# Kernel tuning notes

Hardware: AMD Instinct MI355X
Metric: run time of the kernel (lower is better)

## Reference

```python
import jax, jax.numpy as jnp
import numpy as np

B, D, DEPTH, C = 8192, 2048, 10, 1000
NUM_INNER = 2 ** DEPTH - 1   # 1023
NUM_LEAVES = 2 ** DEPTH      # 1024


def setup_inputs() -> dict:
    key = jax.random.key(0)
    k1, k2, k3, k4 = jax.random.split(key, 4)
    x = jax.random.normal(k1, (B, D), dtype=jnp.float32)
    # scale weights like a typical init so sigmoid isn't fully saturated
    W = jax.random.normal(k2, (D, NUM_INNER), dtype=jnp.float32) * 0.02
    b = jax.random.normal(k3, (NUM_INNER,), dtype=jnp.float32) * 0.02
    leaf_dist = jax.random.normal(k4, (NUM_LEAVES, C), dtype=jnp.float32)
    return {"x": x, "W": W, "b": b, "leaf_dist": leaf_dist}


def reference(x, W, b, leaf_dist):
    # inner node routing probabilities: [B, num_inner]
    decisions = jax.nn.sigmoid(x @ W + b)
    depth = int(np.log2(decisions.shape[1] + 1))
    pp = jnp.ones((x.shape[0], 1), dtype=x.dtype)  # path probs, starts at root
    for d in range(depth):  # small fixed loop over tree depth
        s, e = 2 ** d - 1, 2 ** (d + 1) - 1
        ld = decisions[:, s:e]                      # [B, 2^d]
        pp = jnp.concatenate([pp * ld, pp * (1.0 - ld)], axis=1)  # [B, 2^(d+1)]
        # faithful reproduction of the original's even/odd reordering
        pp = jnp.concatenate([pp[:, ::2], pp[:, 1::2]], axis=1)
    leaf_probs = jax.nn.softmax(leaf_dist, axis=1)  # [num_leaves, C]
    return pp @ leaf_probs                          # [B, C]
```

## Files before the change

kernel.cpp:

```cpp
#include <hip/hip_runtime.h>

typedef __attribute__((ext_vector_type(8))) unsigned short ushort8v;
typedef __attribute__((ext_vector_type(8))) __bf16 bf16x8;
typedef __attribute__((ext_vector_type(4))) float floatx4;

__device__ __forceinline__ unsigned short f2b(float f) {
    unsigned u = __float_as_uint(f);
    unsigned r = u + 0x7fffu + ((u >> 16) & 1u);
    return (unsigned short)(r >> 16);
}
__device__ __forceinline__ float b2f(unsigned short h) {
    return __uint_as_float(((unsigned)h) << 16);
}

__device__ __forceinline__ void gload16(const unsigned short* g, unsigned short* l) {
    __builtin_amdgcn_global_load_lds(
        (const __attribute__((address_space(1))) unsigned int*)g,
        (__attribute__((address_space(3))) unsigned int*)l,
        16, 0, 0);
}


__global__ __launch_bounds__(256) void prep_kernel(const float* __restrict__ x,
                                                   unsigned short* __restrict__ A2x,
                                                   const float* __restrict__ W,
                                                   unsigned short* __restrict__ B2w,
                                                   const float* __restrict__ ld_,
                                                   unsigned short* __restrict__ B2p) {
    __shared__ float tile[32 * 33];
    __shared__ float buf[1000];
    __shared__ float red[8];
    const int b = blockIdx.x, t = threadIdx.x;
    if (b < 2048) {
        const int mt = b >> 2, kq = (b & 3) * 64;
        const int kco = t >> 4, l16 = t & 15;
        const float* xr0 = x + (size_t)(mt * 16 + l16) * 2048;
#pragma unroll
        for (int i = 0; i < 4; i++) {
            const int kc = kq + i * 16 + kco;
            const float* xr = xr0 + kc * 8;
            float4 v0 = *(const float4*)xr;
            float4 v1 = *(const float4*)(xr + 4);
            ushort8v o;
            o[0] = f2b(v0.x); o[1] = f2b(v0.y); o[2] = f2b(v0.z); o[3] = f2b(v0.w);
            o[4] = f2b(v1.x); o[5] = f2b(v1.y); o[6] = f2b(v1.z); o[7] = f2b(v1.w);
            *(ushort8v*)(A2x + ((size_t)(mt * 256 + kc) * 16 + l16) * 8) = o;
        }
    } else if (b < 4096) {
        const int idx = b - 2048;
        const int n0 = (idx & 31) * 32, k0 = (idx >> 5) * 32;
        const int tx = t & 31, ty = t >> 5;
#pragma unroll
        for (int i = 0; i < 4; i++) {
            int k = k0 + ty + i * 8, n = n0 + tx;
            tile[(ty + i * 8) * 33 + tx] = (n < 1023) ? W[(size_t)k * 1023 + n] : 0.f;
        }
        __syncthreads();
#pragma unroll
        for (int i = 0; i < 4; i++) {
            int n = n0 + ty + i * 8, k = k0 + tx;
            size_t off = ((size_t)((n >> 4) * 256 + (k >> 3)) * 16 + (n & 15)) * 8 + (k & 7);
            B2w[off] = f2b(tile[tx * 33 + ty + i * 8]);
        }
    } else {
        const int l0 = b - 4096;
        const float* r = ld_ + (size_t)l0 * 1000;
        float mx = -3.4e38f;
        for (int i = t; i < 1000; i += 256) { float v = r[i]; buf[i] = v; mx = fmaxf(mx, v); }
#pragma unroll
        for (int o = 32; o > 0; o >>= 1) mx = fmaxf(mx, __shfl_down(mx, o));
        if ((t & 63) == 0) red[t >> 6] = mx;
        __syncthreads();
        mx = fmaxf(fmaxf(red[0], red[1]), fmaxf(red[2], red[3]));
        float s = 0.f;
        for (int i = t; i < 1000; i += 256) { float e = __expf(buf[i] - mx); buf[i] = e; s += e; }
#pragma unroll
        for (int o = 32; o > 0; o >>= 1) s += __shfl_down(s, o);
        if ((t & 63) == 0) red[4 + (t >> 6)] = s;
        __syncthreads();
        float inv = 1.f / (red[4] + red[5] + red[6] + red[7]);
        for (int i = t; i < 1024; i += 256) {
            float pv = (i < 1000) ? buf[i] * inv : 0.f;
            size_t off = ((size_t)((i >> 4) * 128 + (l0 >> 3)) * 16 + (i & 15)) * 8 + (l0 & 7);
            B2p[off] = f2b(pv);
        }
    }
}

__global__ __launch_bounds__(256) void pp_kernel(const unsigned short* __restrict__ dec,
                                                 unsigned short* __restrict__ A2p) {
    __shared__ unsigned short dsh[8 * 1024];
    __shared__ float pa[8 * 1024];
    __shared__ float pb[8 * 1024];
    const int t = threadIdx.x;
    const int r0 = blockIdx.x * 8;
    {
        const ushort8v* src = (const ushort8v*)(dec + (size_t)r0 * 1024);
        ushort8v* dst = (ushort8v*)dsh;
        for (int g = t; g < 1024; g += 256) dst[g] = src[g];
    }
    if (t < 8) pa[t * 1024] = 1.f;
    __syncthreads();
    float* cur = pa; float* nxt = pb;
    for (int dep = 0; dep < 10; dep++) {
        const int half = 1 << dep;
        const int len  = half << 1;
        const int total = len << 3;
        for (int idx = t; idx < total; idx += 256) {
            const int r = idx >> (dep + 1);
            const int j = idx & (len - 1);
            int tt = j >> dep;
            int s  = j & (half - 1);
            int i2 = 2 * s + tt;
            int u  = i2 >> dep;
            int rr = i2 & (half - 1);
            float dv = b2f(dsh[r * 1024 + half - 1 + rr]);
            nxt[r * 1024 + j] = cur[r * 1024 + rr] * (u ? (1.f - dv) : dv);
        }
        __syncthreads();
        float* tmp = cur; cur = nxt; nxt = tmp;
    }
    for (int i = t; i < 8192; i += 256) {
        const int r = i >> 10, j = i & 1023;
        const int rrow = r0 + r;
        size_t off = ((size_t)((rrow >> 4) * 128 + (j >> 3)) * 16 + (rrow & 15)) * 8 + (j & 7);
        A2p[off] = f2b(cur[r * 1024 + j]);
    }
}

#define VMW(N) asm volatile("s_waitcnt vmcnt(" #N ")" ::: "memory")

#define P4_STEP(ks_, b_, VM_, DOSTAGE_)                                             \
    {                                                                               \
        VMW(VM_);                                                                   \
        __builtin_amdgcn_s_barrier();                                               \
        __builtin_amdgcn_sched_barrier(0);                                          \
        const unsigned short* lA = &lds[(b_)][0];                                   \
        const unsigned short* lB = &lds[(b_)][4096];                                \
        bf16x8 af[4], bv[4];                                                        \
        _Pragma("unroll")                                                           \
        for (int m2 = 0; m2 < 4; m2++)                                              \
            af[m2] = __builtin_bit_cast(bf16x8,                                     \
                *(const ushort8v*)&lA[((wr * 4 + m2) * 4 + quad) * 128 + l16 * 8]); \
        _Pragma("unroll")                                                           \
        for (int n2 = 0; n2 < 4; n2++)                                              \
            bv[n2] = __builtin_bit_cast(bf16x8,                                     \
                *(const ushort8v*)&lB[((wc * 4 + n2) * 4 + quad) * 128 + l16 * 8]); \
        asm volatile("s_waitcnt lgkmcnt(0)" ::: "memory");                          \
        __builtin_amdgcn_sched_barrier(0);                                          \
        __builtin_amdgcn_s_barrier();                                               \
        __builtin_amdgcn_sched_barrier(0);                                          \
        if (DOSTAGE_) STAGE((ks_) + 4, (b_));                                       \
        __builtin_amdgcn_s_setprio(1);                                              \
        _Pragma("unroll")                                                           \
        for (int m2 = 0; m2 < 4; m2++)                                              \
            _Pragma("unroll")                                                       \
            for (int n2 = 0; n2 < 4; n2++)                                          \
                acc[m2][n2] = __builtin_amdgcn_mfma_f32_16x16x32_bf16(              \
                    af[m2], bv[n2], acc[m2][n2], 0, 0, 0);                          \
        __builtin_amdgcn_s_setprio(0);                                              \
    }

template <int EPI, int KC>
__global__ __launch_bounds__(256, 2) void gemm_p4(const unsigned short* __restrict__ A2,
                                                  const unsigned short* __restrict__ B2,
                                                  const float* __restrict__ bias,
                                                  unsigned short* __restrict__ obf,
                                                  float* __restrict__ of32, int ldo) {
    __shared__ unsigned short lds[4][8192];

    const int tid  = threadIdx.x;
    const int lane = tid & 63;
    const int wave = tid >> 6;
    const int quad = lane >> 4, l16 = lane & 15;
    const int wr = wave >> 1, wc = wave & 1;

    const int bid = blockIdx.x;
    const int bn  = bid & 7;
    const int bm  = bid >> 3;

    const int c0  = tid >> 4;
    const int sub = (tid & 15) * 8;
    const unsigned short* gA0 = A2 + ((size_t)(bm * 8 + (c0 >> 2))        * KC + (c0 & 3)) * 128 + sub;
    const unsigned short* gA1 = A2 + ((size_t)(bm * 8 + ((c0 + 16) >> 2)) * KC + (c0 & 3)) * 128 + sub;
    const unsigned short* gB0 = B2 + ((size_t)(bn * 8 + (c0 >> 2))        * KC + (c0 & 3)) * 128 + sub;
    const unsigned short* gB1 = B2 + ((size_t)(bn * 8 + ((c0 + 16) >> 2)) * KC + (c0 & 3)) * 128 + sub;
    const int dA0 = c0 * 128 + sub;
    const int dA1 = (c0 + 16) * 128 + sub;
    const int dB0 = 4096 + c0 * 128 + sub;
    const int dB1 = 4096 + (c0 + 16) * 128 + sub;

    floatx4 acc[4][4] = {};
    constexpr int nks = KC / 4;

    auto STAGE = [&](int ks, int b) {
        const size_t ko = (size_t)ks * 512;
        gload16(gA0 + ko, &lds[b][dA0]);
        gload16(gA1 + ko, &lds[b][dA1]);
        gload16(gB0 + ko, &lds[b][dB0]);
        gload16(gB1 + ko, &lds[b][dB1]);
    };

    STAGE(0, 0); STAGE(1, 1); STAGE(2, 2); STAGE(3, 3);

    for (int ks = 0; ks < nks - 4; ++ks) {
        P4_STEP(ks, ks & 3, 12, true);
    }
    P4_STEP(nks - 4, (nks - 4) & 3, 12, false);
    P4_STEP(nks - 3, (nks - 3) & 3, 8,  false);
    P4_STEP(nks - 2, (nks - 2) & 3, 4,  false);
    P4_STEP(nks - 1, (nks - 1) & 3, 0,  false);

    const int mt0 = bm * 8 + wr * 4;
    const int nt0 = bn * 8 + wc * 4;
#pragma unroll
    for (int n2 = 0; n2 < 4; n2++) {
        const int col = (nt0 + n2) * 16 + l16;
        float bbias = 0.f;
        if constexpr (EPI == 0) bbias = (col < 1023) ? bias[col] : 0.f;
#pragma unroll
        for (int m2 = 0; m2 < 4; m2++) {
            const int row0 = (mt0 + m2) * 16 + quad * 4;
#pragma unroll
            for (int r = 0; r < 4; r++) {
                float v = acc[m2][n2][r];
                if constexpr (EPI == 0) {
                    float sgm = 1.f / (1.f + __expf(-(v + bbias)));
                    obf[(size_t)(row0 + r) * ldo + col] = f2b(sgm);
                } else {
                    if (col < 1000) of32[(size_t)(row0 + r) * ldo + col] = v;
                }
            }
        }
    }
}

extern "C" void kernel_launch(void* const* d_in, const int* in_sizes, int n_in,
                              void* d_out, int out_size, void* d_ws, size_t ws_size,
                              hipStream_t stream) {
    const float* x   = (const float*)d_in[0];
    const float* W   = (const float*)d_in[1];
    const float* b   = (const float*)d_in[2];
    const float* ldd = (const float*)d_in[3];
    float* out = (float*)d_out;

    char* ws = (char*)d_ws;
    unsigned short* A2x = (unsigned short*)(ws);
    unsigned short* A2p = (unsigned short*)(ws);
    unsigned short* B2w = (unsigned short*)(ws + 33554432);
    unsigned short* dec = (unsigned short*)(ws + 37748736);
    unsigned short* B2p = (unsigned short*)(ws + 54525952);

    prep_kernel<<<5120, 256, 0, stream>>>(x, A2x, W, B2w, ldd, B2p);
    gemm_p4<0, 256><<<512, 256, 0, stream>>>(A2x, B2w, b, dec, nullptr, 1024);
    pp_kernel<<<1024, 256, 0, stream>>>(dec, A2p);
    gemm_p4<1, 128><<<512, 256, 0, stream>>>(A2p, B2p, nullptr, nullptr, out, 1000);
}
```

Before: 210.3 us.

## Use 256x128 tile, 512-thread GEMM with triple buffering and XCD-aware block mapping

Replaces the first GEMM (x@W with sigmoid epilogue) with a new 512-thread kernel using 256x128 tiles and a three-stage LDS ring buffer, halving the grid to 256 blocks with one block per CU. Block indices are remapped so each XCD works on a contiguous group of M-tiles, which should improve L2 reuse of A. The second GEMM gets the same XCD-aware mapping and loses the unused sigmoid epilogue template. The aim is more operand reuse per LDS load and less global traffic. The trade-off is lower occupancy and a shallower prefetch pipeline.

```diff
diff --git a/kernel.cpp b/kernel.cpp
--- a/kernel.cpp
+++ b/kernel.cpp
@@ -13,7 +13,7 @@
     return __uint_as_float(((unsigned)h) << 16);
 }
 
-__device__ __forceinline__ void gload16(const unsigned short* g, unsigned short* l) {
+__device__ __forceinline__ void gload16(const void* g, void* l) {
     __builtin_amdgcn_global_load_lds(
         (const __attribute__((address_space(1))) unsigned int*)g,
         (__attribute__((address_space(3))) unsigned int*)l,
@@ -129,6 +129,102 @@
 }
 
 #define VMW(N) asm volatile("s_waitcnt vmcnt(" #N ")" ::: "memory")
+
+#define M1_STEP(ks_, CUR_, STG_, VM_, DOSTAGE_)                                       \
+    {                                                                                 \
+        if (DOSTAGE_) STAGE((ks_) + 2, (STG_));                                       \
+        VMW(VM_);                                                                     \
+        __builtin_amdgcn_s_barrier();                                                 \
+        const unsigned short* lA = &lds[(CUR_)][0];                                   \
+        const unsigned short* lB = &lds[(CUR_)][8192];                                \
+        bf16x8 af[4], bv[4];                                                          \
+        _Pragma("unroll")                                                             \
+        for (int m2 = 0; m2 < 4; m2++)                                                \
+            af[m2] = __builtin_bit_cast(bf16x8,                                       \
+                *(const ushort8v*)&lA[((wr * 4 + m2) * 4 + quad) * 128 + l16 * 8]);   \
+        _Pragma("unroll")                                                             \
+        for (int n2 = 0; n2 < 4; n2++)                                                \
+            bv[n2] = __builtin_bit_cast(bf16x8,                                       \
+                *(const ushort8v*)&lB[((wc * 4 + n2) * 4 + quad) * 128 + l16 * 8]);   \
+        asm volatile("s_waitcnt lgkmcnt(0)" ::: "memory");                            \
+        __builtin_amdgcn_sched_barrier(0);                                            \
+        __builtin_amdgcn_s_setprio(1);                                                \
+        _Pragma("unroll")                                                             \
+        for (int m2 = 0; m2 < 4; m2++)                                                \
+            _Pragma("unroll")                                                         \
+            for (int n2 = 0; n2 < 4; n2++)                                            \
+                acc[m2][n2] = __builtin_amdgcn_mfma_f32_16x16x32_bf16(                \
+                    af[m2], bv[n2], acc[m2][n2], 0, 0, 0);                            \
+        __builtin_amdgcn_s_setprio(0);                                                \
+        __builtin_amdgcn_s_barrier();                                                 \
+    }
+
+__global__ __launch_bounds__(512, 1) void gemm_m1(const unsigned short* __restrict__ A2,
+                                                  const unsigned short* __restrict__ B2,
+                                                  const float* __restrict__ bias,
+                                                  unsigned short* __restrict__ obf) {
+    constexpr int KC = 256;
+    __shared__ unsigned short lds[3][12288];
+
+    const int tid  = threadIdx.x;
+    const int lane = tid & 63;
+    const int wave = tid >> 6;
+    const int quad = lane >> 4, l16 = lane & 15;
+    const int wr = wave >> 1, wc = wave & 1;
+
+    const int bid = blockIdx.x;
+    const int xcd = bid & 7;
+    const int j   = bid >> 3;
+    const int bm  = xcd * 4 + (j & 3);
+    const int bn  = j >> 2;
+
+    const int cA  = tid >> 4;
+    const int sub = (tid & 15) * 8;
+    const unsigned short* gA0 = A2 + ((size_t)(bm * 16 + (cA >> 2))        * KC + (cA & 3)) * 128 + sub;
+    const unsigned short* gA1 = A2 + ((size_t)(bm * 16 + ((cA + 32) >> 2)) * KC + (cA & 3)) * 128 + sub;
+    const unsigned short* gB0 = B2 + ((size_t)(bn * 8  + (cA >> 2))        * KC + (cA & 3)) * 128 + sub;
+    const int dA0 = cA * 128 + sub;
+    const int dA1 = (cA + 32) * 128 + sub;
+    const int dB0 = 8192 + cA * 128 + sub;
+
+    floatx4 acc[4][4] = {};
+    constexpr int nks = KC / 4;
+
+    auto STAGE = [&](int ks, int b) {
+        const size_t ko = (size_t)ks * 512;
+        gload16(gA0 + ko, &lds[b][dA0]);
+        gload16(gA1 + ko, &lds[b][dA1]);
+        gload16(gB0 + ko, &lds[b][dB0]);
+    };
+
+    STAGE(0, 0); STAGE(1, 1);
+
+    int c0 = 0, c1 = 1, c2 = 2;
+    for (int ks = 0; ks < nks - 2; ++ks) {
+        M1_STEP(ks, c0, c2, 6, true);
+        int tmp = c0; c0 = c1; c1 = c2; c2 = tmp;
+    }
+    M1_STEP(nks - 2, c0, c2, 3, false);
+    { int tmp = c0; c0 = c1; c1 = c2; c2 = tmp; }
+    M1_STEP(nks - 1, c0, c2, 0, false);
+
+    const int mt0 = bm * 16 + wr * 4;
+    const int nt0 = bn * 8  + wc * 4;
+#pragma unroll
+    for (int n2 = 0; n2 < 4; n2++) {
+        const int col = (nt0 + n2) * 16 + l16;
+        const float bbias = (col < 1023) ? bias[col] : 0.f;
+#pragma unroll
+        for (int m2 = 0; m2 < 4; m2++) {
+            const int row0 = (mt0 + m2) * 16 + quad * 4;
+#pragma unroll
+            for (int r = 0; r < 4; r++) {
+                float sgm = 1.f / (1.f + __expf(-(acc[m2][n2][r] + bbias)));
+                obf[(size_t)(row0 + r) * 1024 + col] = f2b(sgm);
+            }
+        }
+    }
+}
 
 #define P4_STEP(ks_, b_, VM_, DOSTAGE_)                                             \
     {                                                                               \
@@ -161,11 +257,9 @@
         __builtin_amdgcn_s_setprio(0);                                              \
     }
 
-template <int EPI, int KC>
+template <int KC>
 __global__ __launch_bounds__(256, 2) void gemm_p4(const unsigned short* __restrict__ A2,
                                                   const unsigned short* __restrict__ B2,
-                                                  const float* __restrict__ bias,
-                                                  unsigned short* __restrict__ obf,
                                                   float* __restrict__ of32, int ldo) {
     __shared__ unsigned short lds[4][8192];
 
@@ -176,8 +270,10 @@
     const int wr = wave >> 1, wc = wave & 1;
 
     const int bid = blockIdx.x;
-    const int bn  = bid & 7;
-    const int bm  = bid >> 3;
+    const int xcd = bid & 7;
+    const int j   = bid >> 3;
+    const int bm  = xcd * 8 + (j & 7);
+    const int bn  = j >> 3;
 
     const int c0  = tid >> 4;
     const int sub = (tid & 15) * 8;
@@ -216,20 +312,12 @@
 #pragma unroll
     for (int n2 = 0; n2 < 4; n2++) {
         const int col = (nt0 + n2) * 16 + l16;
-        float bbias = 0.f;
-        if constexpr (EPI == 0) bbias = (col < 1023) ? bias[col] : 0.f;
 #pragma unroll
         for (int m2 = 0; m2 < 4; m2++) {
             const int row0 = (mt0 + m2) * 16 + quad * 4;
 #pragma unroll
             for (int r = 0; r < 4; r++) {
-                float v = acc[m2][n2][r];
-                if constexpr (EPI == 0) {
-                    float sgm = 1.f / (1.f + __expf(-(v + bbias)));
-                    obf[(size_t)(row0 + r) * ldo + col] = f2b(sgm);
-                } else {
-                    if (col < 1000) of32[(size_t)(row0 + r) * ldo + col] = v;
-                }
+                if (col < 1000) of32[(size_t)(row0 + r) * ldo + col] = acc[m2][n2][r];
             }
         }
     }
@@ -252,7 +340,7 @@
     unsigned short* B2p = (unsigned short*)(ws + 54525952);
 
     prep_kernel<<<5120, 256, 0, stream>>>(x, A2x, W, B2w, ldd, B2p);
-    gemm_p4<0, 256><<<512, 256, 0, stream>>>(A2x, B2w, b, dec, nullptr, 1024);
+    gemm_m1<<<256, 512, 0, stream>>>(A2x, B2w, b, dec);
     pp_kernel<<<1024, 256, 0, stream>>>(dec, A2p);
-    gemm_p4<1, 128><<<512, 256, 0, stream>>>(A2p, B2p, nullptr, nullptr, out, 1000);
-}
+    gemm_p4<128><<<512, 256, 0, stream>>>(A2p, B2p, out, 1000);
+}
```

Measured after the change: 199.8 us. 5.0% less time.
